# Kernel tuning notes

Measured on AMD Instinct MI355X. Metric: run time of the kernel, lower is better.

Reference implementation:

```python
import jax, jax.numpy as jnp
import numpy as np

B, S, D, H = 2, 2048, 1024, 16
HD = D // H  # head_dim = 64


def setup_inputs() -> dict:
    key = jax.random.key(0)
    ks = jax.random.split(key, 9)
    s_in = 1.0 / np.sqrt(D)
    inp = {
        "hidden_state": jax.random.normal(ks[0], (B, S, D), dtype=jnp.float32),
        # per-head projections, stacked: [H, D, HD]
        "Wq": jax.random.uniform(ks[1], (H, D, HD), jnp.float32, -s_in, s_in),
        "bq": jax.random.uniform(ks[2], (H, HD), jnp.float32, -s_in, s_in),
        "Wk": jax.random.uniform(ks[3], (H, D, HD), jnp.float32, -s_in, s_in),
        "bk": jax.random.uniform(ks[4], (H, HD), jnp.float32, -s_in, s_in),
        "Wv": jax.random.uniform(ks[5], (H, D, HD), jnp.float32, -s_in, s_in),
        "bv": jax.random.uniform(ks[6], (H, HD), jnp.float32, -s_in, s_in),
        # output linear: [D, D]
        "Wo": jax.random.uniform(ks[7], (D, D), jnp.float32, -s_in, s_in),
        "bo": jax.random.uniform(ks[8], (D,), jnp.float32, -s_in, s_in),
    }
    return inp


def reference(hidden_state, Wq, bq, Wk, bk, Wv, bv, Wo, bo):
    # fused per-head projections: [B, H, S, HD]
    q = jnp.einsum("bsd,hde->bhse", hidden_state, Wq) + bq[None, :, None, :]
    k = jnp.einsum("bsd,hde->bhse", hidden_state, Wk) + bk[None, :, None, :]
    v = jnp.einsum("bsd,hde->bhse", hidden_state, Wv) + bv[None, :, None, :]
    scale = 1.0 / jnp.sqrt(jnp.float32(HD))
    scores = jnp.einsum("bhse,bhte->bhst", q, k) * scale  # [B, H, S, S]
    weights = jax.nn.softmax(scores, axis=-1)
    ctx = jnp.einsum("bhst,bhte->bhse", weights, v)       # [B, H, S, HD]
    # concat heads along last dim -> [B, S, D]
    ctx = jnp.transpose(ctx, (0, 2, 1, 3)).reshape(B, S, D)
    return ctx @ Wo + bo
```

## Files before the change

kernel.cpp:

```cpp
#include <hip/hip_runtime.h>
#include <hip/hip_bf16.h>
#include <math.h>

#define BB 2
#define SS 2048
#define DD 1024
#define HH 16
#define HD 64

typedef __attribute__((ext_vector_type(8))) _Float16 f16x8;
typedef __attribute__((ext_vector_type(2))) __fp16 fp16x2;
typedef __attribute__((ext_vector_type(8))) unsigned short u16x8;
typedef __attribute__((ext_vector_type(4))) float f32x4;
typedef __attribute__((ext_vector_type(4))) unsigned short u16x4;

__device__ __forceinline__ unsigned short hbits(_Float16 h) {
    union { _Float16 h; unsigned short s; } u; u.h = h; return u.s;
}

__device__ __forceinline__ int swz(int row, int grp) {
    return (row << 6) + (((grp) ^ (row & 7)) << 3);
}

__device__ __forceinline__ float fexp2(float x) {
#if __has_builtin(__builtin_amdgcn_exp2f)
    return __builtin_amdgcn_exp2f(x);
#else
    return exp2f(x);
#endif
}

__device__ __forceinline__ u16x4 pack4(float p0, float p1, float p2, float p3) {
#if __has_builtin(__builtin_amdgcn_cvt_pkrtz)
    union { fp16x2 h[2]; u16x4 u; } pu;
    pu.h[0] = __builtin_amdgcn_cvt_pkrtz(p0, p1);
    pu.h[1] = __builtin_amdgcn_cvt_pkrtz(p2, p3);
    return pu.u;
#else
    u16x4 r;
    r[0] = hbits((_Float16)p0); r[1] = hbits((_Float16)p1);
    r[2] = hbits((_Float16)p2); r[3] = hbits((_Float16)p3);
    return r;
#endif
}

__device__ __forceinline__ void gload_lds16(const unsigned short* g, unsigned short* l) {
#if __has_builtin(__builtin_amdgcn_global_load_lds)
    auto gp = (const __attribute__((address_space(1))) unsigned int*)(uintptr_t)g;
    auto lp = (__attribute__((address_space(3))) unsigned int*)(uintptr_t)l;
    __builtin_amdgcn_global_load_lds(gp, lp, 16, 0, 0);
#else
    *(u16x8*)(l + (threadIdx.x & 63) * 8) = *(const u16x8*)g;
#endif
}

__device__ __forceinline__ void wait4_barrier() {
    asm volatile("s_waitcnt vmcnt(4) lgkmcnt(0)\n\ts_barrier" ::: "memory");
}
__device__ __forceinline__ void wait6_barrier() {
    asm volatile("s_waitcnt vmcnt(6) lgkmcnt(0)\n\ts_barrier" ::: "memory");
}
__device__ __forceinline__ void wait0_barrier() {
    asm volatile("s_waitcnt vmcnt(0) lgkmcnt(0)\n\ts_barrier" ::: "memory");
}

__global__ __launch_bounds__(256) void prep_convert(
    const float* __restrict__ X,
    const float* __restrict__ Wq, const float* __restrict__ Wk,
    const float* __restrict__ Wv, const float* __restrict__ Wo,
    unsigned short* __restrict__ Xh, unsigned short* __restrict__ WT)
{
    __shared__ __align__(16) unsigned short LT[64 * 68];
    const int bid = blockIdx.x;
    const int tid = threadIdx.x;

    if (bid < 2048) {
        const int base = bid * 2048 + tid * 8;
        float4 a = *(const float4*)&X[base];
        float4 b = *(const float4*)&X[base + 4];
        u16x8 o;
        o[0] = hbits((_Float16)a.x); o[1] = hbits((_Float16)a.y);
        o[2] = hbits((_Float16)a.z); o[3] = hbits((_Float16)a.w);
        o[4] = hbits((_Float16)b.x); o[5] = hbits((_Float16)b.y);
        o[6] = hbits((_Float16)b.z); o[7] = hbits((_Float16)b.w);
        *(u16x8*)&Xh[base] = o;
        return;
    }

    const int t = bid - 2048;
    const float* src;
    size_t stride;
    int outRow0, kcol0;
    if (t < 768) {
        const int nt = t >> 4, ktile = t & 15;
        const int sel = nt >> 4, hh = nt & 15;
        const float* Ws = (sel == 0) ? Wq : ((sel == 1) ? Wk : Wv);
        src = Ws + (size_t)hh * (DD * HD) + (size_t)ktile * 64 * HD;
        stride = HD;
        outRow0 = nt * 64;
        kcol0 = ktile * 64;
    } else {
        const int tt = t - 768;
        const int nt = tt & 15, ktile = tt >> 4;
        src = Wo + (size_t)ktile * 64 * DD + nt * 64;
        stride = DD;
        outRow0 = 3072 + nt * 64;
        kcol0 = ktile * 64;
    }

    const int e = tid & 63, dq = tid >> 6;
#pragma unroll
    for (int p = 0; p < 16; p++) {
        const int dl = p * 4 + dq;
        LT[e * 68 + dl] = hbits((_Float16)src[(size_t)dl * stride + e]);
    }
    __syncthreads();
    const int eo = tid >> 2, d16 = (tid & 3) * 16;
#pragma unroll
    for (int j = 0; j < 4; j++) {
        *(ushort4*)&WT[(size_t)(outRow0 + eo) * DD + kcol0 + d16 + j * 4] =
            *(const ushort4*)&LT[eo * 68 + d16 + j * 4];
    }
}

#define GBM 128
#define GBN 128
#define GBK 64
#define NKT (DD / GBK)
#define QBK 32
#define QNKT (DD / QBK)

__global__ __launch_bounds__(256, 3) void qkv_gemm(
    const unsigned short* __restrict__ Xh, const unsigned short* __restrict__ WT,
    const float* __restrict__ bq, const float* __restrict__ bk,
    const float* __restrict__ bv,
    unsigned short* __restrict__ qh, unsigned short* __restrict__ kh,
    unsigned short* __restrict__ vTs, unsigned int* __restrict__ kc2)
{
    __shared__ __align__(16) unsigned short As[3][8 * 512];
    __shared__ __align__(16) unsigned short Bs[3][8 * 512];

    const int tid = threadIdx.x;
    const int m0 = blockIdx.y * GBM;
    const int n0 = blockIdx.x * GBN;
    const int lane = tid & 63;
    const int w = tid >> 6;
    const int wm = w & 1, wn = w >> 1;
    const int l15 = lane & 15, quad = lane >> 4;

    int g_off[2];
#pragma unroll
    for (int p = 0; p < 2; p++) {
        const int c = p * 4 + w;
        g_off[p] = (c * 16 + l15) * DD + quad * 8;
    }

    f32x4 acc[4][4];
#pragma unroll
    for (int i = 0; i < 4; i++)
#pragma unroll
        for (int j = 0; j < 4; j++) acc[i][j] = (f32x4){0.f, 0.f, 0.f, 0.f};

    const unsigned short* Abase = Xh + (size_t)m0 * DD;
    const unsigned short* Bbase = WT + (size_t)n0 * DD;

#pragma unroll
    for (int p = 0; p < 2; p++) {
        gload_lds16(Abase + g_off[p], &As[0][(p * 4 + w) * 512]);
        gload_lds16(Bbase + g_off[p], &Bs[0][(p * 4 + w) * 512]);
    }
#pragma unroll
    for (int p = 0; p < 2; p++) {
        gload_lds16(Abase + g_off[p] + QBK, &As[1][(p * 4 + w) * 512]);
        gload_lds16(Bbase + g_off[p] + QBK, &Bs[1][(p * 4 + w) * 512]);
    }
    wait0_barrier();

    int cur = 0, pre = 2;
    for (int t = 0; t < QNKT; t++) {
        if (t + 2 < QNKT) {
            const int kt2 = (t + 2) * QBK;
#pragma unroll
            for (int p = 0; p < 2; p++) {
                gload_lds16(Abase + g_off[p] + kt2, &As[pre][(p * 4 + w) * 512]);
                gload_lds16(Bbase + g_off[p] + kt2, &Bs[pre][(p * 4 + w) * 512]);
            }
        }
        f16x8 af[4], bf[4];
#pragma unroll
        for (int i = 0; i < 4; i++) {
            af[i] = *(const f16x8*)&As[cur][(wm * 4 + i) * 512 + lane * 8];
            bf[i] = *(const f16x8*)&Bs[cur][(wn * 4 + i) * 512 + lane * 8];
        }
#pragma unroll
        for (int ns = 0; ns < 4; ns++)
#pragma unroll
            for (int ms = 0; ms < 4; ms++)
                acc[ms][ns] = __builtin_amdgcn_mfma_f32_16x16x32_f16(
                    af[ms], bf[ns], acc[ms][ns], 0, 0, 0);
        if (t < QNKT - 2)       wait4_barrier();
        else if (t == QNKT - 2) wait0_barrier();
        cur = (cur == 2) ? 0 : cur + 1;
        pre = (pre == 2) ? 0 : pre + 1;
    }

    const int sel = n0 >> 10;
    const int hw = ((n0 + wn * 64) >> 6) & 15;
    const int bblk = m0 >> 11;
    const float* bias = (sel == 0) ? bq : ((sel == 1) ? bk : bv);
    const size_t bh_base = ((size_t)bblk * HH + hw) * SS * HD;
    float wmx = 0.0f;
#pragma unroll
    for (int ms = 0; ms < 4; ms++) {
#pragma unroll
        for (int rr = 0; rr < 4; rr++) {
            const int m = m0 + wm * 64 + ms * 16 + quad * 4 + rr;
            const int s = m & (SS - 1);
            const int s63 = s & 63;
            float v2 = 0.0f;
#pragma unroll
            for (int ns = 0; ns < 4; ns++) {
                const int e = ns * 16 + l15;
                const float val = acc[ms][ns][rr] + bias[hw * HD + e];
                if (sel == 0) {
                    qh[bh_base + (size_t)s * HD + e] = hbits((_Float16)val);
                } else if (sel == 1) {
                    v2 = fmaf(val, val, v2);
                    const size_t kofs = bh_base + (size_t)(s >> 6) * 4096
                                      + swz(s63, e >> 3) + (e & 7);
                    kh[kofs] = hbits((_Float16)val);
                } else {
                    const size_t vofs = bh_base + (size_t)(s >> 6) * 4096
                                      + swz(e, s63 >> 3) + (s63 & 7);
                    vTs[vofs] = hbits((_Float16)val);
                }
            }
            if (sel == 1) {
                v2 += __shfl_xor(v2, 1);
                v2 += __shfl_xor(v2, 2);
                v2 += __shfl_xor(v2, 4);
                v2 += __shfl_xor(v2, 8);
                wmx = fmaxf(wmx, v2);
            }
        }
    }
    if (sel == 1) {
        wmx = fmaxf(wmx, __shfl_xor(wmx, 16));
        wmx = fmaxf(wmx, __shfl_xor(wmx, 32));
        if (lane == 0)
            atomicMax(&kc2[bblk * HH + hw], __float_as_uint(wmx));
    }
}

__global__ __launch_bounds__(256, 2) void out_gemm(
    const unsigned short* __restrict__ Ctxh, const unsigned short* __restrict__ WoT,
    const float* __restrict__ bo, float* __restrict__ out)
{
    __shared__ __align__(16) unsigned short As[3][16 * 512];
    __shared__ __align__(16) unsigned short Bs[3][8 * 512];

    const int tid = threadIdx.x;
    const int f  = blockIdx.y * 16 + blockIdx.x;
    const int fs = (f & 7) * 64 + (f >> 3);
    const int bx = fs % 16, by = fs / 16;
    const int m0 = by * 128;
    const int n0 = bx * 64;
    const int lane = tid & 63;
    const int w = tid >> 6;
    const int wm = w & 1, wn = w >> 1;
    const int l15 = lane & 15, quad = lane >> 4;

    int g_off[4];
#pragma unroll
    for (int p = 0; p < 4; p++) {
        const int c = p * 4 + w;
        g_off[p] = ((c >> 1) * 16 + l15) * DD + (c & 1) * 32 + quad * 8;
    }

    f32x4 acc[4][2];
#pragma unroll
    for (int i = 0; i < 4; i++)
#pragma unroll
        for (int j = 0; j < 2; j++) acc[i][j] = (f32x4){0.f, 0.f, 0.f, 0.f};

    const unsigned short* Abase = Ctxh + (size_t)m0 * DD;
    const unsigned short* Bbase = WoT + (size_t)n0 * DD;

#pragma unroll
    for (int p = 0; p < 4; p++)
        gload_lds16(Abase + g_off[p], &As[0][(p * 4 + w) * 512]);
#pragma unroll
    for (int p = 0; p < 2; p++)
        gload_lds16(Bbase + g_off[p], &Bs[0][(p * 4 + w) * 512]);
#pragma unroll
    for (int p = 0; p < 4; p++)
        gload_lds16(Abase + g_off[p] + GBK, &As[1][(p * 4 + w) * 512]);
#pragma unroll
    for (int p = 0; p < 2; p++)
        gload_lds16(Bbase + g_off[p] + GBK, &Bs[1][(p * 4 + w) * 512]);
    wait0_barrier();

    int cur = 0, pre = 2;
    for (int it = 0; it < NKT; it++) {
        if (it + 2 < NKT) {
            const int kt2 = (it + 2) * GBK;
#pragma unroll
            for (int p = 0; p < 4; p++)
                gload_lds16(Abase + g_off[p] + kt2, &As[pre][(p * 4 + w) * 512]);
#pragma unroll
            for (int p = 0; p < 2; p++)
                gload_lds16(Bbase + g_off[p] + kt2, &Bs[pre][(p * 4 + w) * 512]);
        }
#pragma unroll
        for (int ks = 0; ks < 2; ks++) {
            f16x8 af[4], bf[2];
#pragma unroll
            for (int i = 0; i < 4; i++)
                af[i] = *(const f16x8*)&As[cur][((wm * 4 + i) * 2 + ks) * 512 + lane * 8];
#pragma unroll
            for (int j = 0; j < 2; j++)
                bf[j] = *(const f16x8*)&Bs[cur][((wn * 2 + j) * 2 + ks) * 512 + lane * 8];
#pragma unroll
            for (int ns = 0; ns < 2; ns++)
#pragma unroll
                for (int ms = 0; ms < 4; ms++)
                    acc[ms][ns] = __builtin_amdgcn_mfma_f32_16x16x32_f16(
                        af[ms], bf[ns], acc[ms][ns], 0, 0, 0);
        }
        if (it < NKT - 2)       wait6_barrier();
        else if (it == NKT - 2) wait0_barrier();
        cur = (cur == 2) ? 0 : cur + 1;
        pre = (pre == 2) ? 0 : pre + 1;
    }

#pragma unroll
    for (int ms = 0; ms < 4; ms++) {
#pragma unroll
        for (int rr = 0; rr < 4; rr++) {
            const size_t m = (size_t)(m0 + wm * 64 + ms * 16 + quad * 4 + rr);
#pragma unroll
            for (int ns = 0; ns < 2; ns++) {
                const int n = n0 + wn * 32 + ns * 16 + l15;
                out[m * DD + n] = acc[ms][ns][rr] + bo[n];
            }
        }
    }
}

#define TQB 128
#define TKB 64
#define NT (SS / TKB)
#define C1 0.1803368801111204f

__global__ __launch_bounds__(256, 2) void attn_mfma(
    const unsigned short* __restrict__ qh, const unsigned short* __restrict__ kh,
    const unsigned short* __restrict__ vTs, const unsigned int* __restrict__ kc2,
    unsigned short* __restrict__ ctxh)
{
    __shared__ __align__(16) unsigned short KL [3][TKB * 64];
    __shared__ __align__(16) unsigned short VtL[3][HD * 64];
    __shared__ __align__(16) unsigned short PsL[4][32 * 64];

    const int tid  = threadIdx.x;
    const int lane = tid & 63;
    const int w    = tid >> 6;
    const int l15  = lane & 15;
    const int quad = lane >> 4;
    const int f  = blockIdx.y * 16 + blockIdx.x;
    const int fs = (f & 7) * 64 + (f >> 3);
    const int bh = fs >> 4;
    const int q0 = (fs & 15) * TQB;

    const float kfac = sqrtf(__uint_as_float(kc2[bh])) * 1.01f * C1;

    f16x8 qf[2][2];
    float M2[2];
#pragma unroll
    for (int msub = 0; msub < 2; msub++) {
        const unsigned short* qrow =
            qh + ((size_t)bh * SS + q0 + w * 32 + msub * 16 + l15) * HD;
        float nq2 = 0.0f;
#pragma unroll
        for (int dstep = 0; dstep < 2; dstep++) {
            qf[msub][dstep] = *(const f16x8*)&qrow[dstep * 32 + quad * 8];
#pragma unroll
            for (int j = 0; j < 8; j++) {
                const float x = (float)qf[msub][dstep][j];
                nq2 = fmaf(x, x, nq2);
            }
        }
        nq2 += __shfl_xor(nq2, 16);
        nq2 += __shfl_xor(nq2, 32);
        M2[msub] = sqrtf(nq2) * kfac;
    }

    f16x8 ones;
#pragma unroll
    for (int j = 0; j < 8; j++) ones[j] = (_Float16)1.0f;

    f32x4 o[2][4], lones[2];
#pragma unroll
    for (int ms = 0; ms < 2; ms++) {
        lones[ms] = (f32x4){0.f, 0.f, 0.f, 0.f};
#pragma unroll
        for (int e = 0; e < 4; e++) o[ms][e] = (f32x4){0.f, 0.f, 0.f, 0.f};
    }

    const unsigned short* kb0 = kh  + (size_t)bh * SS * HD;
    const unsigned short* vb0 = vTs + (size_t)bh * SS * HD;

    gload_lds16(kb0 + tid * 8,        &KL [0][w * 512]);
    gload_lds16(kb0 + 2048 + tid * 8, &KL [0][2048 + w * 512]);
    gload_lds16(vb0 + tid * 8,        &VtL[0][w * 512]);
    gload_lds16(vb0 + 2048 + tid * 8, &VtL[0][2048 + w * 512]);
    gload_lds16(kb0 + 4096 + tid * 8, &KL [1][w * 512]);
    gload_lds16(kb0 + 6144 + tid * 8, &KL [1][2048 + w * 512]);
    gload_lds16(vb0 + 4096 + tid * 8, &VtL[1][w * 512]);
    gload_lds16(vb0 + 6144 + tid * 8, &VtL[1][2048 + w * 512]);
    wait0_barrier();

    int cur = 0, pre = 2;
    for (int t = 0; t < NT; t++) {
        if (t + 2 < NT) {
            const unsigned short* kb = kb0 + (size_t)(t + 2) * 4096;
            const unsigned short* vb = vb0 + (size_t)(t + 2) * 4096;
            gload_lds16(kb + tid * 8,        &KL [pre][w * 512]);
            gload_lds16(kb + 2048 + tid * 8, &KL [pre][2048 + w * 512]);
            gload_lds16(vb + tid * 8,        &VtL[pre][w * 512]);
            gload_lds16(vb + 2048 + tid * 8, &VtL[pre][2048 + w * 512]);
        }

        f32x4 sc[2][4];
        __builtin_amdgcn_s_setprio(1);
#pragma unroll
        for (int ksub = 0; ksub < 4; ksub++) {
            const int row = ksub * 16 + l15;
            f16x8 k0 = *(const f16x8*)&KL[cur][swz(row, quad)];
            f16x8 k1 = *(const f16x8*)&KL[cur][swz(row, 4 + quad)];
#pragma unroll
            for (int msub = 0; msub < 2; msub++) {
                f32x4 a = (f32x4){0.f, 0.f, 0.f, 0.f};
                a = __builtin_amdgcn_mfma_f32_16x16x32_f16(k0, qf[msub][0], a, 0, 0, 0);
                a = __builtin_amdgcn_mfma_f32_16x16x32_f16(k1, qf[msub][1], a, 0, 0, 0);
                sc[msub][ksub] = a;
            }
        }
        __builtin_amdgcn_s_setprio(0);

#pragma unroll
        for (int msub = 0; msub < 2; msub++) {
            const int prow = msub * 16 + l15;
#pragma unroll
            for (int ksub = 0; ksub < 4; ksub++) {
                const float p0 = fexp2(fmaf(sc[msub][ksub][0], C1, -M2[msub]));
                const float p1 = fexp2(fmaf(sc[msub][ksub][1], C1, -M2[msub]));
                const float p2 = fexp2(fmaf(sc[msub][ksub][2], C1, -M2[msub]));
                const float p3 = fexp2(fmaf(sc[msub][ksub][3], C1, -M2[msub]));
                *(u16x4*)&PsL[w][swz(prow, ksub * 2 + (quad >> 1)) + (quad & 1) * 4] =
                    pack4(p0, p1, p2, p3);
            }
        }

        __builtin_amdgcn_s_setprio(1);
#pragma unroll
        for (int kj = 0; kj < 2; kj++) {
            f16x8 pa[2];
#pragma unroll
            for (int msub = 0; msub < 2; msub++)
                pa[msub] = *(const f16x8*)&PsL[w][swz(msub * 16 + l15, kj * 4 + quad)];
            lones[0] = __builtin_amdgcn_mfma_f32_16x16x32_f16(pa[0], ones, lones[0], 0, 0, 0);
            lones[1] = __builtin_amdgcn_mfma_f32_16x16x32_f16(pa[1], ones, lones[1], 0, 0, 0);
#pragma unroll
            for (int esub = 0; esub < 4; esub++) {
                f16x8 vr = *(const f16x8*)&VtL[cur][swz(esub * 16 + l15, kj * 4 + quad)];
                o[0][esub] = __builtin_amdgcn_mfma_f32_16x16x32_f16(pa[0], vr, o[0][esub], 0, 0, 0);
                o[1][esub] = __builtin_amdgcn_mfma_f32_16x16x32_f16(pa[1], vr, o[1][esub], 0, 0, 0);
            }
        }
        __builtin_amdgcn_s_setprio(0);

        if (t < NT - 2)       wait4_barrier();
        else if (t == NT - 2) wait0_barrier();
        cur = (cur == 2) ? 0 : cur + 1;
        pre = (pre == 2) ? 0 : pre + 1;
    }

    const int b = bh >> 4;
    const int h = bh & 15;
#pragma unroll
    for (int msub = 0; msub < 2; msub++) {
#pragma unroll
        for (int rr = 0; rr < 4; rr++) {
            const float linv = 1.0f / lones[msub][rr];
            const int row = q0 + w * 32 + msub * 16 + quad * 4 + rr;
#pragma unroll
            for (int esub = 0; esub < 4; esub++) {
                ctxh[((size_t)b * SS + row) * DD + h * HD + esub * 16 + l15] =
                    hbits((_Float16)(o[msub][esub][rr] * linv));
            }
        }
    }
}

extern "C" void kernel_launch(void* const* d_in, const int* in_sizes, int n_in,
                              void* d_out, int out_size, void* d_ws, size_t ws_size,
                              hipStream_t stream) {
    const float* X  = (const float*)d_in[0];
    const float* Wq = (const float*)d_in[1];
    const float* bq = (const float*)d_in[2];
    const float* Wk = (const float*)d_in[3];
    const float* bk = (const float*)d_in[4];
    const float* Wv = (const float*)d_in[5];
    const float* bv = (const float*)d_in[6];
    const float* Wo = (const float*)d_in[7];
    const float* bo = (const float*)d_in[8];
    float* out = (float*)d_out;

    const size_t NB2 = (size_t)4096 * 1024 * 2;
    unsigned char* w8 = (unsigned char*)d_ws;
    unsigned short* Xh   = (unsigned short*)(w8);
    unsigned short* WT   = (unsigned short*)(w8 + NB2);
    unsigned short* qh   = (unsigned short*)(w8 + 2 * NB2);
    unsigned short* kh   = (unsigned short*)(w8 + 3 * NB2);
    unsigned short* vTs  = (unsigned short*)(w8 + 4 * NB2);
    unsigned short* ctxh = (unsigned short*)(w8 + 5 * NB2);
    unsigned int*   kc2  = (unsigned int*)(w8 + 6 * NB2);
    unsigned short* WoT  = WT + (size_t)3072 * 1024;

    (void)hipMemsetAsync(kc2, 0, BB * HH * sizeof(unsigned int), stream);

    prep_convert<<<dim3(3072), 256, 0, stream>>>(X, Wq, Wk, Wv, Wo, Xh, WT);

    qkv_gemm<<<dim3(3072 / GBN, 4096 / GBM), 256, 0, stream>>>(
        Xh, WT, bq, bk, bv, qh, kh, vTs, kc2);

    attn_mfma<<<dim3(SS / TQB, BB * HH), 256, 0, stream>>>(qh, kh, vTs, kc2, ctxh);

    out_gemm<<<dim3(1024 / 64, 4096 / 128), 256, 0, stream>>>(ctxh, WoT, bo, out);
}
```

Baseline: 222.8 us.

## Restructure QKV GEMM into per-head blocks with warp-private LDS pipelines

Each QKV GEMM block now computes the Q, K and V tiles for a single head over 128 rows, instead of one 128-column slice of the concatenated projection. Each warp stages its own A and B sub-tiles into private LDS buffers with double buffering and waits only on its own vmcnt, which removes the block-wide barriers from the main loop. Because a warp now holds only half of a head's columns, the K row norms for the attention scaling max are summed through LDS atomics before one atomicMax per block. In exchange, each A tile is loaded twice, once per column-warp, the grid shrinks from 768 to 512 blocks, and occupancy is lowered to 2 blocks per CU.

```diff
diff --git a/kernel.cpp b/kernel.cpp
--- a/kernel.cpp
+++ b/kernel.cpp
@@ -130,125 +130,130 @@
 #define QBK 32
 #define QNKT (DD / QBK)
 
-__global__ __launch_bounds__(256, 3) void qkv_gemm(
+__global__ __launch_bounds__(256, 2) void qkv_gemm(
     const unsigned short* __restrict__ Xh, const unsigned short* __restrict__ WT,
     const float* __restrict__ bq, const float* __restrict__ bk,
     const float* __restrict__ bv,
     unsigned short* __restrict__ qh, unsigned short* __restrict__ kh,
     unsigned short* __restrict__ vTs, unsigned int* __restrict__ kc2)
 {
-    __shared__ __align__(16) unsigned short As[3][8 * 512];
-    __shared__ __align__(16) unsigned short Bs[3][8 * 512];
-
-    const int tid = threadIdx.x;
-    const int m0 = blockIdx.y * GBM;
-    const int n0 = blockIdx.x * GBN;
+    __shared__ __align__(16) unsigned short AW[4][2][2048];
+    __shared__ __align__(16) unsigned short BW[4][3][2][1024];
+
+    const int tid  = threadIdx.x;
     const int lane = tid & 63;
-    const int w = tid >> 6;
-    const int wm = w & 1, wn = w >> 1;
-    const int l15 = lane & 15, quad = lane >> 4;
-
-    int g_off[2];
-#pragma unroll
-    for (int p = 0; p < 2; p++) {
-        const int c = p * 4 + w;
-        g_off[p] = (c * 16 + l15) * DD + quad * 8;
-    }
-
-    f32x4 acc[4][4];
-#pragma unroll
-    for (int i = 0; i < 4; i++)
-#pragma unroll
-        for (int j = 0; j < 4; j++) acc[i][j] = (f32x4){0.f, 0.f, 0.f, 0.f};
-
-    const unsigned short* Abase = Xh + (size_t)m0 * DD;
-    const unsigned short* Bbase = WT + (size_t)n0 * DD;
-
-#pragma unroll
-    for (int p = 0; p < 2; p++) {
-        gload_lds16(Abase + g_off[p], &As[0][(p * 4 + w) * 512]);
-        gload_lds16(Bbase + g_off[p], &Bs[0][(p * 4 + w) * 512]);
-    }
-#pragma unroll
-    for (int p = 0; p < 2; p++) {
-        gload_lds16(Abase + g_off[p] + QBK, &As[1][(p * 4 + w) * 512]);
-        gload_lds16(Bbase + g_off[p] + QBK, &Bs[1][(p * 4 + w) * 512]);
-    }
-    wait0_barrier();
-
-    int cur = 0, pre = 2;
+    const int w    = tid >> 6;
+    const int wm   = w & 1, wn = w >> 1;
+    const int l15  = lane & 15, quad = lane >> 4;
+    const int m0   = blockIdx.y * 128;
+    const int head = blockIdx.x;
+
+    const unsigned short* Ab = Xh + (size_t)(m0 + wm * 64) * DD;
+    const unsigned short* Bb = WT + (size_t)(head * 64 + wn * 32) * DD;
+
+    int aoff[4], boff[2];
+#pragma unroll
+    for (int c = 0; c < 4; c++) aoff[c] = (c * 16 + l15) * DD + quad * 8;
+#pragma unroll
+    for (int c = 0; c < 2; c++) boff[c] = (c * 16 + l15) * DD + quad * 8;
+
+    f32x4 acc[3][4][2];
+#pragma unroll
+    for (int s = 0; s < 3; s++)
+#pragma unroll
+        for (int i = 0; i < 4; i++)
+#pragma unroll
+            for (int j = 0; j < 2; j++) acc[s][i][j] = (f32x4){0.f, 0.f, 0.f, 0.f};
+
+    auto STAGE = [&](int b, int ke) {
+#pragma unroll
+        for (int c = 0; c < 4; c++)
+            gload_lds16(Ab + aoff[c] + ke, &AW[w][b][c * 512]);
+#pragma unroll
+        for (int sel = 0; sel < 3; sel++)
+#pragma unroll
+            for (int c = 0; c < 2; c++)
+                gload_lds16(Bb + (size_t)sel * 1024 * DD + boff[c] + ke,
+                            &BW[w][sel][b][c * 512]);
+    };
+
+    STAGE(0, 0);
+    STAGE(1, QBK);
+    asm volatile("s_waitcnt vmcnt(10)" ::: "memory");
+
     for (int t = 0; t < QNKT; t++) {
-        if (t + 2 < QNKT) {
-            const int kt2 = (t + 2) * QBK;
-#pragma unroll
-            for (int p = 0; p < 2; p++) {
-                gload_lds16(Abase + g_off[p] + kt2, &As[pre][(p * 4 + w) * 512]);
-                gload_lds16(Bbase + g_off[p] + kt2, &Bs[pre][(p * 4 + w) * 512]);
-            }
-        }
-        f16x8 af[4], bf[4];
-#pragma unroll
-        for (int i = 0; i < 4; i++) {
-            af[i] = *(const f16x8*)&As[cur][(wm * 4 + i) * 512 + lane * 8];
-            bf[i] = *(const f16x8*)&Bs[cur][(wn * 4 + i) * 512 + lane * 8];
-        }
-#pragma unroll
-        for (int ns = 0; ns < 4; ns++)
+        const int b = t & 1;
+        f16x8 af[4], bf[3][2];
+#pragma unroll
+        for (int ms = 0; ms < 4; ms++)
+            af[ms] = *(const f16x8*)&AW[w][b][ms * 512 + lane * 8];
+#pragma unroll
+        for (int sel = 0; sel < 3; sel++)
+#pragma unroll
+            for (int ns = 0; ns < 2; ns++)
+                bf[sel][ns] = *(const f16x8*)&BW[w][sel][b][ns * 512 + lane * 8];
+        asm volatile("s_waitcnt lgkmcnt(0)" ::: "memory");
+        __builtin_amdgcn_sched_barrier(0);
+        if (t + 2 < QNKT) STAGE(b, (t + 2) * QBK);
+#pragma unroll
+        for (int sel = 0; sel < 3; sel++)
 #pragma unroll
             for (int ms = 0; ms < 4; ms++)
-                acc[ms][ns] = __builtin_amdgcn_mfma_f32_16x16x32_f16(
-                    af[ms], bf[ns], acc[ms][ns], 0, 0, 0);
-        if (t < QNKT - 2)       wait4_barrier();
-        else if (t == QNKT - 2) wait0_barrier();
-        cur = (cur == 2) ? 0 : cur + 1;
-        pre = (pre == 2) ? 0 : pre + 1;
-    }
-
-    const int sel = n0 >> 10;
-    const int hw = ((n0 + wn * 64) >> 6) & 15;
+#pragma unroll
+                for (int ns = 0; ns < 2; ns++)
+                    acc[sel][ms][ns] = __builtin_amdgcn_mfma_f32_16x16x32_f16(
+                        af[ms], bf[sel][ns], acc[sel][ms][ns], 0, 0, 0);
+        if (t < QNKT - 2)       asm volatile("s_waitcnt vmcnt(10)" ::: "memory");
+        else if (t == QNKT - 2) asm volatile("s_waitcnt vmcnt(0)"  ::: "memory");
+    }
+
+    __syncthreads();
+    float* rs = (float*)&AW[0][0][0];
+    if (tid < 128) rs[tid] = 0.f;
+    __syncthreads();
+
     const int bblk = m0 >> 11;
-    const float* bias = (sel == 0) ? bq : ((sel == 1) ? bk : bv);
-    const size_t bh_base = ((size_t)bblk * HH + hw) * SS * HD;
-    float wmx = 0.0f;
+    const size_t bh_base = ((size_t)bblk * HH + head) * (size_t)SS * HD;
+
 #pragma unroll
     for (int ms = 0; ms < 4; ms++) {
 #pragma unroll
         for (int rr = 0; rr < 4; rr++) {
-            const int m = m0 + wm * 64 + ms * 16 + quad * 4 + rr;
-            const int s = m & (SS - 1);
-            const int s63 = s & 63;
+            const int rloc = wm * 64 + ms * 16 + quad * 4 + rr;
+            const int s    = (m0 + rloc) & (SS - 1);
+            const int s63  = s & 63;
             float v2 = 0.0f;
 #pragma unroll
-            for (int ns = 0; ns < 4; ns++) {
-                const int e = ns * 16 + l15;
-                const float val = acc[ms][ns][rr] + bias[hw * HD + e];
-                if (sel == 0) {
-                    qh[bh_base + (size_t)s * HD + e] = hbits((_Float16)val);
-                } else if (sel == 1) {
-                    v2 = fmaf(val, val, v2);
-                    const size_t kofs = bh_base + (size_t)(s >> 6) * 4096
-                                      + swz(s63, e >> 3) + (e & 7);
-                    kh[kofs] = hbits((_Float16)val);
-                } else {
-                    const size_t vofs = bh_base + (size_t)(s >> 6) * 4096
-                                      + swz(e, s63 >> 3) + (s63 & 7);
-                    vTs[vofs] = hbits((_Float16)val);
-                }
-            }
-            if (sel == 1) {
-                v2 += __shfl_xor(v2, 1);
-                v2 += __shfl_xor(v2, 2);
-                v2 += __shfl_xor(v2, 4);
-                v2 += __shfl_xor(v2, 8);
-                wmx = fmaxf(wmx, v2);
-            }
-        }
-    }
-    if (sel == 1) {
-        wmx = fmaxf(wmx, __shfl_xor(wmx, 16));
-        wmx = fmaxf(wmx, __shfl_xor(wmx, 32));
+            for (int ns = 0; ns < 2; ns++) {
+                const int e = wn * 32 + ns * 16 + l15;
+                const float vq = acc[0][ms][ns][rr] + bq[head * HD + e];
+                qh[bh_base + (size_t)s * HD + e] = hbits((_Float16)vq);
+                const float vk = acc[1][ms][ns][rr] + bk[head * HD + e];
+                v2 = fmaf(vk, vk, v2);
+                kh[bh_base + (size_t)(s >> 6) * 4096 + swz(s63, e >> 3) + (e & 7)] =
+                    hbits((_Float16)vk);
+                const float vv = acc[2][ms][ns][rr] + bv[head * HD + e];
+                vTs[bh_base + (size_t)(s >> 6) * 4096 + swz(e, s63 >> 3) + (s63 & 7)] =
+                    hbits((_Float16)vv);
+            }
+            v2 += __shfl_xor(v2, 1);
+            v2 += __shfl_xor(v2, 2);
+            v2 += __shfl_xor(v2, 4);
+            v2 += __shfl_xor(v2, 8);
+            if (l15 == 0) atomicAdd(&rs[rloc], v2);
+        }
+    }
+    __syncthreads();
+    if (w == 0) {
+        float mx = fmaxf(rs[lane], rs[64 + lane]);
+        mx = fmaxf(mx, __shfl_xor(mx, 1));
+        mx = fmaxf(mx, __shfl_xor(mx, 2));
+        mx = fmaxf(mx, __shfl_xor(mx, 4));
+        mx = fmaxf(mx, __shfl_xor(mx, 8));
+        mx = fmaxf(mx, __shfl_xor(mx, 16));
+        mx = fmaxf(mx, __shfl_xor(mx, 32));
         if (lane == 0)
-            atomicMax(&kc2[bblk * HH + hw], __float_as_uint(wmx));
+            atomicMax(&kc2[bblk * HH + head], __float_as_uint(mx));
     }
 }
 
@@ -531,7 +536,7 @@
 
     prep_convert<<<dim3(3072), 256, 0, stream>>>(X, Wq, Wk, Wv, Wo, Xh, WT);
 
-    qkv_gemm<<<dim3(3072 / GBN, 4096 / GBM), 256, 0, stream>>>(
+    qkv_gemm<<<dim3(HH, 4096 / 128), 256, 0, stream>>>(
         Xh, WT, bq, bk, bv, qh, kh, vTs, kc2);
 
     attn_mfma<<<dim3(SS / TQB, BB * HH), 256, 0, stream>>>(qh, kh, vTs, kc2, ctxh);
```

Result: slower. 242.2 us (+8.7%).

## Switch QKV GEMM to 32x32x16 MFMA with fragment-packed X and W layouts

Applied to the files above, without the earlier changes.

The prep kernel now writes X and the Q/K/V weights in a pre-packed fragment layout: 32-row by 16-k blocks of 512 halves, in the order each lane needs. The QKV GEMM can then stage each block with one contiguous wave-wide load and feed 32x32x16 MFMAs instead of 16x16x32 ones. This is meant to cut LDS fragment reads per MFMA and make global-to-LDS copies contiguous. In exchange, the epilogue must follow the 32x32 accumulator row mapping, the K-norm reduction shuffles change, and the X conversion goes through LDS.

```diff
diff --git a/kernel.cpp b/kernel.cpp
--- a/kernel.cpp
+++ b/kernel.cpp
@@ -12,6 +12,7 @@
 typedef __attribute__((ext_vector_type(2))) __fp16 fp16x2;
 typedef __attribute__((ext_vector_type(8))) unsigned short u16x8;
 typedef __attribute__((ext_vector_type(4))) float f32x4;
+typedef __attribute__((ext_vector_type(16))) float f32x16;
 typedef __attribute__((ext_vector_type(4))) unsigned short u16x4;
 
 __device__ __forceinline__ unsigned short hbits(_Float16 h) {
@@ -68,58 +69,83 @@
     const float* __restrict__ X,
     const float* __restrict__ Wq, const float* __restrict__ Wk,
     const float* __restrict__ Wv, const float* __restrict__ Wo,
-    unsigned short* __restrict__ Xh, unsigned short* __restrict__ WT)
+    unsigned short* __restrict__ Xh2, unsigned short* __restrict__ WT)
 {
     __shared__ __align__(16) unsigned short LT[64 * 68];
     const int bid = blockIdx.x;
     const int tid = threadIdx.x;
 
     if (bid < 2048) {
-        const int base = bid * 2048 + tid * 8;
-        float4 a = *(const float4*)&X[base];
-        float4 b = *(const float4*)&X[base + 4];
-        u16x8 o;
-        o[0] = hbits((_Float16)a.x); o[1] = hbits((_Float16)a.y);
-        o[2] = hbits((_Float16)a.z); o[3] = hbits((_Float16)a.w);
-        o[4] = hbits((_Float16)b.x); o[5] = hbits((_Float16)b.y);
-        o[6] = hbits((_Float16)b.z); o[7] = hbits((_Float16)b.w);
-        *(u16x8*)&Xh[base] = o;
+        const int mblk = bid >> 4;
+        const int kg   = bid & 15;
+        {
+            const int r  = tid >> 3;
+            const int c0 = (tid & 7) * 8;
+            const float* src = X + (size_t)(mblk * 32 + r) * DD + kg * 64 + c0;
+            float4 a = *(const float4*)src;
+            float4 b = *(const float4*)(src + 4);
+            unsigned short* d = &LT[r * 68 + c0];
+            d[0] = hbits((_Float16)a.x); d[1] = hbits((_Float16)a.y);
+            d[2] = hbits((_Float16)a.z); d[3] = hbits((_Float16)a.w);
+            d[4] = hbits((_Float16)b.x); d[5] = hbits((_Float16)b.y);
+            d[6] = hbits((_Float16)b.z); d[7] = hbits((_Float16)b.w);
+        }
+        __syncthreads();
+        const int fbl = tid >> 6, l = tid & 63;
+        const int row = l & 31, c = fbl * 16 + (l >> 5) * 8;
+        u16x8 v = *(const u16x8*)&LT[row * 68 + c];
+        *(u16x8*)&Xh2[((size_t)mblk * 64 + kg * 4 + fbl) * 512 + l * 8] = v;
         return;
     }
 
     const int t = bid - 2048;
-    const float* src;
-    size_t stride;
-    int outRow0, kcol0;
     if (t < 768) {
         const int nt = t >> 4, ktile = t & 15;
         const int sel = nt >> 4, hh = nt & 15;
         const float* Ws = (sel == 0) ? Wq : ((sel == 1) ? Wk : Wv);
-        src = Ws + (size_t)hh * (DD * HD) + (size_t)ktile * 64 * HD;
-        stride = HD;
-        outRow0 = nt * 64;
-        kcol0 = ktile * 64;
+        const float* src = Ws + (size_t)hh * (DD * HD) + (size_t)ktile * 64 * HD;
+        const int outRow0 = nt * 64;
+        const int kcol0   = ktile * 64;
+
+        const int e = tid & 63, dq = tid >> 6;
+#pragma unroll
+        for (int p = 0; p < 16; p++) {
+            const int dl = p * 4 + dq;
+            LT[e * 68 + dl] = hbits((_Float16)src[(size_t)dl * HD + e]);
+        }
+        __syncthreads();
+#pragma unroll
+        for (int p = 0; p < 2; p++) {
+            const int sidx = p * 2048 + tid * 8;
+            const int fb = sidx >> 9;
+            const int l  = (sidx >> 3) & 63;
+            const int nb = fb >> 2, kb = fb & 3;
+            const int ee = nb * 32 + (l & 31);
+            const int dl = kb * 16 + (l >> 5) * 8;
+            u16x8 v = *(const u16x8*)&LT[ee * 68 + dl];
+            *(u16x8*)&WT[(((size_t)(outRow0 >> 5) + nb) * 64 + (kcol0 >> 4) + kb) * 512
+                         + l * 8] = v;
+        }
     } else {
         const int tt = t - 768;
         const int nt = tt & 15, ktile = tt >> 4;
-        src = Wo + (size_t)ktile * 64 * DD + nt * 64;
-        stride = DD;
-        outRow0 = 3072 + nt * 64;
-        kcol0 = ktile * 64;
-    }
-
-    const int e = tid & 63, dq = tid >> 6;
-#pragma unroll
-    for (int p = 0; p < 16; p++) {
-        const int dl = p * 4 + dq;
-        LT[e * 68 + dl] = hbits((_Float16)src[(size_t)dl * stride + e]);
-    }
-    __syncthreads();
-    const int eo = tid >> 2, d16 = (tid & 3) * 16;
-#pragma unroll
-    for (int j = 0; j < 4; j++) {
-        *(ushort4*)&WT[(size_t)(outRow0 + eo) * DD + kcol0 + d16 + j * 4] =
-            *(const ushort4*)&LT[eo * 68 + d16 + j * 4];
+        const float* src = Wo + (size_t)ktile * 64 * DD + nt * 64;
+        const int outRow0 = 3072 + nt * 64;
+        const int kcol0 = ktile * 64;
+
+        const int e = tid & 63, dq = tid >> 6;
+#pragma unroll
+        for (int p = 0; p < 16; p++) {
+            const int dl = p * 4 + dq;
+            LT[e * 68 + dl] = hbits((_Float16)src[(size_t)dl * DD + e]);
+        }
+        __syncthreads();
+        const int eo = tid >> 2, d16 = (tid & 3) * 16;
+#pragma unroll
+        for (int j = 0; j < 4; j++) {
+            *(ushort4*)&WT[(size_t)(outRow0 + eo) * DD + kcol0 + d16 + j * 4] =
+                *(const ushort4*)&LT[eo * 68 + d16 + j * 4];
+        }
     }
 }
 
@@ -131,7 +157,7 @@
 #define QNKT (DD / QBK)
 
 __global__ __launch_bounds__(256, 3) void qkv_gemm(
-    const unsigned short* __restrict__ Xh, const unsigned short* __restrict__ WT,
+    const unsigned short* __restrict__ Xh2, const unsigned short* __restrict__ WT2,
     const float* __restrict__ bq, const float* __restrict__ bk,
     const float* __restrict__ bv,
     unsigned short* __restrict__ qh, unsigned short* __restrict__ kh,
@@ -140,64 +166,71 @@
     __shared__ __align__(16) unsigned short As[3][8 * 512];
     __shared__ __align__(16) unsigned short Bs[3][8 * 512];
 
-    const int tid = threadIdx.x;
-    const int m0 = blockIdx.y * GBM;
-    const int n0 = blockIdx.x * GBN;
+    const int tid  = threadIdx.x;
+    const int m0   = blockIdx.y * GBM;
+    const int n0   = blockIdx.x * GBN;
     const int lane = tid & 63;
-    const int w = tid >> 6;
-    const int wm = w & 1, wn = w >> 1;
-    const int l15 = lane & 15, quad = lane >> 4;
-
-    int g_off[2];
-#pragma unroll
-    for (int p = 0; p < 2; p++) {
-        const int c = p * 4 + w;
-        g_off[p] = (c * 16 + l15) * DD + quad * 8;
-    }
-
-    f32x4 acc[4][4];
-#pragma unroll
-    for (int i = 0; i < 4; i++)
-#pragma unroll
-        for (int j = 0; j < 4; j++) acc[i][j] = (f32x4){0.f, 0.f, 0.f, 0.f};
-
-    const unsigned short* Abase = Xh + (size_t)m0 * DD;
-    const unsigned short* Bbase = WT + (size_t)n0 * DD;
-
-#pragma unroll
-    for (int p = 0; p < 2; p++) {
-        gload_lds16(Abase + g_off[p], &As[0][(p * 4 + w) * 512]);
-        gload_lds16(Bbase + g_off[p], &Bs[0][(p * 4 + w) * 512]);
-    }
-#pragma unroll
-    for (int p = 0; p < 2; p++) {
-        gload_lds16(Abase + g_off[p] + QBK, &As[1][(p * 4 + w) * 512]);
-        gload_lds16(Bbase + g_off[p] + QBK, &Bs[1][(p * 4 + w) * 512]);
-    }
+    const int w    = tid >> 6;
+    const int wm   = w & 1, wn = w >> 1;
+    const int l31  = lane & 31, h = lane >> 5;
+
+    f32x16 acc[2][2];
+#pragma unroll
+    for (int i = 0; i < 2; i++)
+#pragma unroll
+        for (int j = 0; j < 2; j++)
+#pragma unroll
+            for (int k = 0; k < 16; k++) acc[i][j][k] = 0.f;
+
+    const size_t mb0 = (size_t)(m0 >> 5);
+    const size_t nb0 = (size_t)(n0 >> 5);
+
+    auto STAGE = [&](int buf, int t) {
+#pragma unroll
+        for (int p = 0; p < 4; p++) {
+            const int c = p * 4 + w;
+            const unsigned short* src;
+            unsigned short* dst;
+            if (c < 8) {
+                src = Xh2 + ((mb0 + (c >> 1)) * 64 + t * 2 + (c & 1)) * 512 + lane * 8;
+                dst = &As[buf][c * 512];
+            } else {
+                const int d = c - 8;
+                src = WT2 + ((nb0 + (d >> 1)) * 64 + t * 2 + (d & 1)) * 512 + lane * 8;
+                dst = &Bs[buf][d * 512];
+            }
+            gload_lds16(src, dst);
+        }
+    };
+
+    STAGE(0, 0);
+    STAGE(1, 1);
     wait0_barrier();
 
     int cur = 0, pre = 2;
     for (int t = 0; t < QNKT; t++) {
-        if (t + 2 < QNKT) {
-            const int kt2 = (t + 2) * QBK;
-#pragma unroll
-            for (int p = 0; p < 2; p++) {
-                gload_lds16(Abase + g_off[p] + kt2, &As[pre][(p * 4 + w) * 512]);
-                gload_lds16(Bbase + g_off[p] + kt2, &Bs[pre][(p * 4 + w) * 512]);
-            }
-        }
-        f16x8 af[4], bf[4];
-#pragma unroll
-        for (int i = 0; i < 4; i++) {
-            af[i] = *(const f16x8*)&As[cur][(wm * 4 + i) * 512 + lane * 8];
-            bf[i] = *(const f16x8*)&Bs[cur][(wn * 4 + i) * 512 + lane * 8];
-        }
-#pragma unroll
-        for (int ns = 0; ns < 4; ns++)
-#pragma unroll
-            for (int ms = 0; ms < 4; ms++)
-                acc[ms][ns] = __builtin_amdgcn_mfma_f32_16x16x32_f16(
-                    af[ms], bf[ns], acc[ms][ns], 0, 0, 0);
+        if (t + 2 < QNKT) STAGE(pre, t + 2);
+        f16x8 af[2][2], bf[2][2];
+#pragma unroll
+        for (int mi = 0; mi < 2; mi++)
+#pragma unroll
+            for (int kb = 0; kb < 2; kb++)
+                af[mi][kb] = *(const f16x8*)
+                    &As[cur][(((wm * 2 + mi) << 1) + kb) * 512 + lane * 8];
+#pragma unroll
+        for (int ni = 0; ni < 2; ni++)
+#pragma unroll
+            for (int kb = 0; kb < 2; kb++)
+                bf[ni][kb] = *(const f16x8*)
+                    &Bs[cur][(((wn * 2 + ni) << 1) + kb) * 512 + lane * 8];
+#pragma unroll
+        for (int kb = 0; kb < 2; kb++)
+#pragma unroll
+            for (int mi = 0; mi < 2; mi++)
+#pragma unroll
+                for (int ni = 0; ni < 2; ni++)
+                    acc[mi][ni] = __builtin_amdgcn_mfma_f32_32x32x16_f16(
+                        af[mi][kb], bf[ni][kb], acc[mi][ni], 0, 0, 0);
         if (t < QNKT - 2)       wait4_barrier();
         else if (t == QNKT - 2) wait0_barrier();
         cur = (cur == 2) ? 0 : cur + 1;
@@ -205,34 +238,32 @@
     }
 
     const int sel = n0 >> 10;
-    const int hw = ((n0 + wn * 64) >> 6) & 15;
+    const int hw  = ((n0 + wn * 64) >> 6) & 15;
     const int bblk = m0 >> 11;
     const float* bias = (sel == 0) ? bq : ((sel == 1) ? bk : bv);
-    const size_t bh_base = ((size_t)bblk * HH + hw) * SS * HD;
+    const size_t bh_base = ((size_t)bblk * HH + hw) * (size_t)SS * HD;
     float wmx = 0.0f;
 #pragma unroll
-    for (int ms = 0; ms < 4; ms++) {
-#pragma unroll
-        for (int rr = 0; rr < 4; rr++) {
-            const int m = m0 + wm * 64 + ms * 16 + quad * 4 + rr;
-            const int s = m & (SS - 1);
+    for (int mi = 0; mi < 2; mi++) {
+#pragma unroll
+        for (int r = 0; r < 16; r++) {
+            const int srow = wm * 64 + mi * 32 + (r & 3) + 8 * (r >> 2) + 4 * h;
+            const int s = (m0 + srow) & (SS - 1);
             const int s63 = s & 63;
             float v2 = 0.0f;
 #pragma unroll
-            for (int ns = 0; ns < 4; ns++) {
-                const int e = ns * 16 + l15;
-                const float val = acc[ms][ns][rr] + bias[hw * HD + e];
+            for (int ni = 0; ni < 2; ni++) {
+                const int e = ni * 32 + l31;
+                const float val = acc[mi][ni][r] + bias[hw * HD + e];
                 if (sel == 0) {
                     qh[bh_base + (size_t)s * HD + e] = hbits((_Float16)val);
                 } else if (sel == 1) {
                     v2 = fmaf(val, val, v2);
-                    const size_t kofs = bh_base + (size_t)(s >> 6) * 4096
-                                      + swz(s63, e >> 3) + (e & 7);
-                    kh[kofs] = hbits((_Float16)val);
+                    kh[bh_base + (size_t)(s >> 6) * 4096 + swz(s63, e >> 3) + (e & 7)] =
+                        hbits((_Float16)val);
                 } else {
-                    const size_t vofs = bh_base + (size_t)(s >> 6) * 4096
-                                      + swz(e, s63 >> 3) + (s63 & 7);
-                    vTs[vofs] = hbits((_Float16)val);
+                    vTs[bh_base + (size_t)(s >> 6) * 4096 + swz(e, s63 >> 3) + (s63 & 7)] =
+                        hbits((_Float16)val);
                 }
             }
             if (sel == 1) {
@@ -240,12 +271,12 @@
                 v2 += __shfl_xor(v2, 2);
                 v2 += __shfl_xor(v2, 4);
                 v2 += __shfl_xor(v2, 8);
+                v2 += __shfl_xor(v2, 16);
                 wmx = fmaxf(wmx, v2);
             }
         }
     }
     if (sel == 1) {
-        wmx = fmaxf(wmx, __shfl_xor(wmx, 16));
         wmx = fmaxf(wmx, __shfl_xor(wmx, 32));
         if (lane == 0)
             atomicMax(&kc2[bblk * HH + hw], __float_as_uint(wmx));
@@ -486,7 +517,7 @@
     }
 
     const int b = bh >> 4;
-    const int h = bh & 15;
+    const int hh = bh & 15;
 #pragma unroll
     for (int msub = 0; msub < 2; msub++) {
 #pragma unroll
@@ -495,7 +526,7 @@
             const int row = q0 + w * 32 + msub * 16 + quad * 4 + rr;
 #pragma unroll
             for (int esub = 0; esub < 4; esub++) {
-                ctxh[((size_t)b * SS + row) * DD + h * HD + esub * 16 + l15] =
+                ctxh[((size_t)b * SS + row) * DD + hh * HD + esub * 16 + l15] =
                     hbits((_Float16)(o[msub][esub][rr] * linv));
             }
         }
@@ -518,7 +549,7 @@
 
     const size_t NB2 = (size_t)4096 * 1024 * 2;
     unsigned char* w8 = (unsigned char*)d_ws;
-    unsigned short* Xh   = (unsigned short*)(w8);
+    unsigned short* Xh2  = (unsigned short*)(w8);
     unsigned short* WT   = (unsigned short*)(w8 + NB2);
     unsigned short* qh   = (unsigned short*)(w8 + 2 * NB2);
     unsigned short* kh   = (unsigned short*)(w8 + 3 * NB2);
@@ -529,10 +560,10 @@
 
     (void)hipMemsetAsync(kc2, 0, BB * HH * sizeof(unsigned int), stream);
 
-    prep_convert<<<dim3(3072), 256, 0, stream>>>(X, Wq, Wk, Wv, Wo, Xh, WT);
+    prep_convert<<<dim3(3072), 256, 0, stream>>>(X, Wq, Wk, Wv, Wo, Xh2, WT);
 
     qkv_gemm<<<dim3(3072 / GBN, 4096 / GBM), 256, 0, stream>>>(
-        Xh, WT, bq, bk, bv, qh, kh, vTs, kc2);
+        Xh2, WT, bq, bk, bv, qh, kh, vTs, kc2);
 
     attn_mfma<<<dim3(SS / TQB, BB * HH), 256, 0, stream>>>(qh, kh, vTs, kc2, ctxh);
 
```

Result: faster. 214.4 us (-3.8%).
